# Performance work log

Hardware: AMD Instinct MI355X
Metric: run time of the kernel (lower is better)

The kernel has to match this reference:

```python
import jax, jax.numpy as jnp
import numpy as np

EPS_POS = 0.65
EPS_NEG = 0.4
TAU = 0.03
TEMPERATURE = 0.07


def setup_inputs() -> dict:
    key = jax.random.key(0)
    k1, k2 = jax.random.split(key)
    N, H, W, C = 256, 14, 14, 512  # ResNet18 layer4 features (448x448 frame), pooled audio
    frame = jax.random.normal(k1, (N, H, W, C), dtype=jnp.float32)
    audio = jax.random.normal(k2, (N, C), dtype=jnp.float32)
    return {"frame": frame, "audio": audio}


def reference(frame, audio):
    # frame: [N, H, W, C] vision backbone features; audio: [N, C] pooled audio embedding
    N = frame.shape[0]
    f = frame * jax.lax.rsqrt(jnp.sum(frame * frame, axis=3, keepdims=True))  # l2_normalize axis=3
    a = audio * jax.lax.rsqrt(jnp.sum(audio * audio, axis=1, keepdims=True))  # l2_normalize axis=1

    # S_ii: per-sample spatial similarity map [N, 1, H, W]
    S_ii = jnp.einsum('nhwc,nc->nhw', f, a)[:, None, :, :]
    # S_ij: cross-batch similarity [N, K, H, W] (K == N)
    S_ij = jnp.einsum('nhwc,kc->nkhw', f, a)

    m_ip = jax.nn.sigmoid((S_ii - EPS_POS) / TAU)   # positive soft-mask
    neg = 1.0 - jax.nn.sigmoid((S_ii - EPS_NEG) / TAU)  # hard-negative soft-mask

    # Pi: masked mean of positive similarities -> [N, 1]
    Pi = jnp.sum(m_ip * S_ii, axis=(2, 3)) / jnp.sum(m_ip, axis=(2, 3))

    n_all = jax.nn.sigmoid((S_ij - EPS_POS) / TAU)
    mask = 1.0 - 100.0 * jnp.eye(N, dtype=frame.dtype)  # kill diagonal (self) pairs
    Ni_easy = (jnp.sum(n_all * S_ij, axis=(2, 3)) / jnp.sum(n_all, axis=(2, 3))) * mask  # [N, N]
    Ni_hard = jnp.sum(neg * S_ii, axis=(2, 3)) / jnp.sum(neg, axis=(2, 3))  # [N, 1]

    data = jnp.concatenate([Pi, Ni_hard, Ni_easy], axis=1) * TEMPERATURE  # [N, N+2]

    # __calc_loss (faithful to TF broadcasting: Pi_d is [N,1], Ni_d is [N] -> [N,N] broadcast)
    Pi_d = data[:, 0:1]
    Ni_d = jnp.sum(data[:, 1:], axis=1)
    Pi_e = jnp.exp(Pi_d)
    Ni_e = jnp.exp(Ni_d)
    loss = (-1.0 / N) * jnp.sum(jnp.log(Pi_e / (Pi_e + Ni_e)))
    return loss
```

## Files before the change

### kernel.cpp

```cpp
#include <hip/hip_runtime.h>
#include <stdint.h>

#define N_IMG 256
#define HW 196
#define CDIM 512

#define F_EPS_POS 0.65f
#define F_EPS_NEG 0.40f
#define F_INV_TAU (1.0f/0.03f)
#define F_TEMP 0.07f

typedef __attribute__((ext_vector_type(8))) short bf16x8;
typedef __attribute__((ext_vector_type(4))) unsigned short u16x4;
typedef __attribute__((ext_vector_type(4))) float f32x4;

__device__ __forceinline__ unsigned short f2bf(float x){
    unsigned int u = __float_as_uint(x);
    u = (u + 0x7FFFu + ((u >> 16) & 1u)) >> 16;
    return (unsigned short)u;
}
__device__ __forceinline__ float sigm(float x){ return 1.0f/(1.0f + __expf(-x)); }

__global__ void audio_norm_k(const float* __restrict__ audio,
                             unsigned short* __restrict__ abf){
    int k = blockIdx.x, t = threadIdx.x;
    __shared__ float red[256];
    float v0 = audio[k*CDIM + t];
    float v1 = audio[k*CDIM + t + 256];
    red[t] = v0*v0 + v1*v1;
    __syncthreads();
    for (int s = 128; s > 0; s >>= 1){
        if (t < s) red[t] += red[t+s];
        __syncthreads();
    }
    float rrt = 1.0f / sqrtf(red[0]);
    abf[k*CDIM + t]       = f2bf(v0*rrt);
    abf[k*CDIM + t + 256] = f2bf(v1*rrt);
}

__global__ __launch_bounds__(512, 2)
void main_k(const float* __restrict__ frame,
            const unsigned short* __restrict__ abf,
            float* __restrict__ num, float* __restrict__ den,
            float* __restrict__ hnum, float* __restrict__ hden){
    __shared__ unsigned short fT[2][16*520];
    __shared__ float rnormS[2][16];

    const int t    = threadIdx.x;
    const int n    = blockIdx.x;
    const int lane = t & 63, wid = t >> 6;
    const int col  = lane & 15, quad = lane >> 4;
    const int kg0  = wid*32 + col;
    const int kg1  = kg0 + 16;

    bf16x8 B0[16], B1[16];
    {
        const unsigned short* b0p = abf + (size_t)kg0*CDIM + quad*8;
        const unsigned short* b1p = abf + (size_t)kg1*CDIM + quad*8;
        #pragma unroll
        for (int j = 0; j < 16; ++j){
            B0[j] = *(const bf16x8*)(b0p + j*32);
            B1[j] = *(const bf16x8*)(b1p + j*32);
        }
    }

    const int r0 = 2*wid, r1 = r0 + 1;

    float en0=0.f, en1=0.f, ed0=0.f, ed1=0.f;
    float hn0=0.f, hn1=0.f, hd0=0.f, hd1=0.f;

    auto loadT = [&](int pt, float4* v){
        int p0 = pt*16 + r0; if (p0 > HW-1) p0 = HW-1;
        int p1 = pt*16 + r1; if (p1 > HW-1) p1 = HW-1;
        const float4* s0 = (const float4*)(frame + ((size_t)n*HW + p0)*CDIM);
        const float4* s1 = (const float4*)(frame + ((size_t)n*HW + p1)*CDIM);
        v[0] = s0[lane]; v[1] = s0[lane + 64];
        v[2] = s1[lane]; v[3] = s1[lane + 64];
    };
    auto storeT = [&](const float4* v, int buf){
        float ss0 = v[0].x*v[0].x + v[0].y*v[0].y + v[0].z*v[0].z + v[0].w*v[0].w
                  + v[1].x*v[1].x + v[1].y*v[1].y + v[1].z*v[1].z + v[1].w*v[1].w;
        float ss1 = v[2].x*v[2].x + v[2].y*v[2].y + v[2].z*v[2].z + v[2].w*v[2].w
                  + v[3].x*v[3].x + v[3].y*v[3].y + v[3].z*v[3].z + v[3].w*v[3].w;
        unsigned short* d0 = fT[buf] + r0*520;
        unsigned short* d1 = fT[buf] + r1*520;
        u16x4 u0 = { f2bf(v[0].x), f2bf(v[0].y), f2bf(v[0].z), f2bf(v[0].w) };
        u16x4 u1 = { f2bf(v[1].x), f2bf(v[1].y), f2bf(v[1].z), f2bf(v[1].w) };
        u16x4 u2 = { f2bf(v[2].x), f2bf(v[2].y), f2bf(v[2].z), f2bf(v[2].w) };
        u16x4 u3 = { f2bf(v[3].x), f2bf(v[3].y), f2bf(v[3].z), f2bf(v[3].w) };
        *(u16x4*)(d0 + lane*4)       = u0;
        *(u16x4*)(d0 + 256 + lane*4) = u1;
        *(u16x4*)(d1 + lane*4)       = u2;
        *(u16x4*)(d1 + 256 + lane*4) = u3;
        #pragma unroll
        for (int d = 1; d < 64; d <<= 1){
            ss0 += __shfl_xor(ss0, d, 64);
            ss1 += __shfl_xor(ss1, d, 64);
        }
        if (lane == 0){
            rnormS[buf][r0] = (ss0 > 0.f) ? (1.0f/sqrtf(ss0)) : 0.f;
            rnormS[buf][r1] = (ss1 > 0.f) ? (1.0f/sqrtf(ss1)) : 0.f;
        }
    };

    {
        float4 v[4];
        loadT(0, v);
        storeT(v, 0);
    }
    __syncthreads();

    for (int pt = 0; pt < 13; ++pt){
        const int cur = pt & 1, nxt = cur ^ 1;
        const bool hasNext = (pt < 12);

        float4 v[4];
        if (hasNext) loadT(pt + 1, v);

        const unsigned short* fbase = fT[cur] + col*520 + quad*8;
        f32x4 acc0 = {0.f,0.f,0.f,0.f};
        f32x4 acc1 = {0.f,0.f,0.f,0.f};
        #pragma unroll
        for (int j = 0; j < 16; ++j){
            bf16x8 a = *(const bf16x8*)(fbase + j*32);
            acc0 = __builtin_amdgcn_mfma_f32_16x16x32_bf16(a, B0[j], acc0, 0, 0, 0);
            acc1 = __builtin_amdgcn_mfma_f32_16x16x32_bf16(a, B1[j], acc1, 0, 0, 0);
        }
        f32x4 rn4 = *(const f32x4*)(&rnormS[cur][quad*4]);
        #pragma unroll
        for (int rr = 0; rr < 4; ++rr){
            int prow = pt*16 + quad*4 + rr;
            if (prow < HW){
                float s0 = acc0[rr] * rn4[rr];
                float s1 = acc1[rr] * rn4[rr];
                float w0 = sigm((s0 - F_EPS_POS) * F_INV_TAU);
                float w1 = sigm((s1 - F_EPS_POS) * F_INV_TAU);
                en0 += w0*s0; ed0 += w0;
                en1 += w1*s1; ed1 += w1;
                if (kg0 == n){ float wn = 1.f - sigm((s0 - F_EPS_NEG) * F_INV_TAU); hn0 += wn*s0; hd0 += wn; }
                if (kg1 == n){ float wn = 1.f - sigm((s1 - F_EPS_NEG) * F_INV_TAU); hn1 += wn*s1; hd1 += wn; }
            }
        }

        if (hasNext) storeT(v, nxt);
        __syncthreads();
    }

    en0 += __shfl_xor(en0, 16, 64); en0 += __shfl_xor(en0, 32, 64);
    ed0 += __shfl_xor(ed0, 16, 64); ed0 += __shfl_xor(ed0, 32, 64);
    en1 += __shfl_xor(en1, 16, 64); en1 += __shfl_xor(en1, 32, 64);
    ed1 += __shfl_xor(ed1, 16, 64); ed1 += __shfl_xor(ed1, 32, 64);
    hn0 += __shfl_xor(hn0, 16, 64); hn0 += __shfl_xor(hn0, 32, 64);
    hd0 += __shfl_xor(hd0, 16, 64); hd0 += __shfl_xor(hd0, 32, 64);
    hn1 += __shfl_xor(hn1, 16, 64); hn1 += __shfl_xor(hn1, 32, 64);
    hd1 += __shfl_xor(hd1, 16, 64); hd1 += __shfl_xor(hd1, 32, 64);

    if (quad == 0){
        num[n*N_IMG + kg0] = en0;  den[n*N_IMG + kg0] = ed0;
        num[n*N_IMG + kg1] = en1;  den[n*N_IMG + kg1] = ed1;
        if (kg0 == n){ hnum[n] = hn0; hden[n] = hd0; }
        if (kg1 == n){ hnum[n] = hn1; hden[n] = hd1; }
    }
}

__global__ void pd_k(const float* __restrict__ num, const float* __restrict__ den,
                     const float* __restrict__ hnum, const float* __restrict__ hden,
                     float* __restrict__ Pi_d, float* __restrict__ Ni_d){
    int nn = blockIdx.x, t = threadIdx.x;
    __shared__ float red[256];
    __shared__ float diagv;
    float ratio = num[nn*N_IMG + t] / den[nn*N_IMG + t];
    if (t == nn) diagv = ratio;
    red[t] = ratio * (t == nn ? -99.f : 1.f);
    __syncthreads();
    for (int s = 128; s > 0; s >>= 1){
        if (t < s) red[t] += red[t+s];
        __syncthreads();
    }
    if (t == 0){
        Pi_d[nn] = F_TEMP * diagv;
        Ni_d[nn] = F_TEMP * (hnum[nn]/hden[nn] + red[0]);
    }
}

__global__ void loss_k(const float* __restrict__ Pi_d, const float* __restrict__ Ni_d,
                       float* __restrict__ out){
    int i = blockIdx.x, j = threadIdx.x;
    __shared__ float red[256];
    float x = Ni_d[j] - Pi_d[i];
    red[j] = (x > 20.f) ? x : log1pf(__expf(x));
    __syncthreads();
    for (int s = 128; s > 0; s >>= 1){
        if (j < s) red[j] += red[j+s];
        __syncthreads();
    }
    if (j == 0) atomicAdd(out, red[0] * (1.0f/(float)N_IMG));
}

extern "C" void kernel_launch(void* const* d_in, const int* in_sizes, int n_in,
                              void* d_out, int out_size, void* d_ws, size_t ws_size,
                              hipStream_t stream) {
    const float* frame = (const float*)d_in[0];
    const float* audio = (const float*)d_in[1];
    float* out = (float*)d_out;
    char* ws = (char*)d_ws;

    unsigned short* abf = (unsigned short*)(ws);
    float* num  = (float*)(ws + 262144);
    float* den  = (float*)(ws + 524288);
    float* hnum = (float*)(ws + 786432);
    float* hden = (float*)(ws + 787456);
    float* Pi_d = (float*)(ws + 788480);
    float* Ni_d = (float*)(ws + 789504);

    hipMemsetAsync(out, 0, sizeof(float), stream);

    audio_norm_k<<<N_IMG, 256, 0, stream>>>(audio, abf);
    main_k<<<N_IMG, 512, 0, stream>>>(frame, abf, num, den, hnum, hden);
    pd_k<<<N_IMG, 256, 0, stream>>>(num, den, hnum, hden, Pi_d, Ni_d);
    loss_k<<<N_IMG, 256, 0, stream>>>(Pi_d, Ni_d, out);
}
```

Baseline: 175.9 us.

## Deepen global prefetch to two tiles and replace syncthreads with LDS-only barrier

The frame tile loop is fully unrolled and uses two register buffers, so global loads for tile pt+2 are issued while tile pt is computed and tile pt+1 is stored to LDS. __syncthreads is replaced by a barrier that waits only on LDS counters, so outstanding global loads do not stall at each barrier. This is meant to hide HBM latency in the memory-bound main kernel. In exchange it raises register pressure under a launch bound of 2 blocks per CU, which could cause spills.

```diff
diff --git a/kernel.cpp b/kernel.cpp
--- a/kernel.cpp
+++ b/kernel.cpp
@@ -69,11 +69,13 @@
     float en0=0.f, en1=0.f, ed0=0.f, ed1=0.f;
     float hn0=0.f, hn1=0.f, hd0=0.f, hd1=0.f;
 
+    const float4* fbase_g = (const float4*)(frame + (size_t)n*HW*CDIM);
+
     auto loadT = [&](int pt, float4* v){
         int p0 = pt*16 + r0; if (p0 > HW-1) p0 = HW-1;
         int p1 = pt*16 + r1; if (p1 > HW-1) p1 = HW-1;
-        const float4* s0 = (const float4*)(frame + ((size_t)n*HW + p0)*CDIM);
-        const float4* s1 = (const float4*)(frame + ((size_t)n*HW + p1)*CDIM);
+        const float4* s0 = fbase_g + (size_t)p0*(CDIM/4);
+        const float4* s1 = fbase_g + (size_t)p1*(CDIM/4);
         v[0] = s0[lane]; v[1] = s0[lane + 64];
         v[2] = s1[lane]; v[3] = s1[lane + 64];
     };
@@ -93,9 +95,9 @@
         *(u16x4*)(d1 + lane*4)       = u2;
         *(u16x4*)(d1 + 256 + lane*4) = u3;
         #pragma unroll
-        for (int d = 1; d < 64; d <<= 1){
-            ss0 += __shfl_xor(ss0, d, 64);
-            ss1 += __shfl_xor(ss1, d, 64);
+        for (int dd = 1; dd < 64; dd <<= 1){
+            ss0 += __shfl_xor(ss0, dd, 64);
+            ss1 += __shfl_xor(ss1, dd, 64);
         }
         if (lane == 0){
             rnormS[buf][r0] = (ss0 > 0.f) ? (1.0f/sqrtf(ss0)) : 0.f;
@@ -103,48 +105,65 @@
         }
     };
 
-    {
-        float4 v[4];
-        loadT(0, v);
-        storeT(v, 0);
-    }
-    __syncthreads();
-
-    for (int pt = 0; pt < 13; ++pt){
-        const int cur = pt & 1, nxt = cur ^ 1;
-        const bool hasNext = (pt < 12);
-
-        float4 v[4];
-        if (hasNext) loadT(pt + 1, v);
-
-        const unsigned short* fbase = fT[cur] + col*520 + quad*8;
-        f32x4 acc0 = {0.f,0.f,0.f,0.f};
-        f32x4 acc1 = {0.f,0.f,0.f,0.f};
-        #pragma unroll
-        for (int j = 0; j < 16; ++j){
-            bf16x8 a = *(const bf16x8*)(fbase + j*32);
-            acc0 = __builtin_amdgcn_mfma_f32_16x16x32_bf16(a, B0[j], acc0, 0, 0, 0);
-            acc1 = __builtin_amdgcn_mfma_f32_16x16x32_bf16(a, B1[j], acc1, 0, 0, 0);
-        }
-        f32x4 rn4 = *(const f32x4*)(&rnormS[cur][quad*4]);
-        #pragma unroll
-        for (int rr = 0; rr < 4; ++rr){
-            int prow = pt*16 + quad*4 + rr;
-            if (prow < HW){
-                float s0 = acc0[rr] * rn4[rr];
-                float s1 = acc1[rr] * rn4[rr];
-                float w0 = sigm((s0 - F_EPS_POS) * F_INV_TAU);
-                float w1 = sigm((s1 - F_EPS_POS) * F_INV_TAU);
-                en0 += w0*s0; ed0 += w0;
-                en1 += w1*s1; ed1 += w1;
-                if (kg0 == n){ float wn = 1.f - sigm((s0 - F_EPS_NEG) * F_INV_TAU); hn0 += wn*s0; hd0 += wn; }
-                if (kg1 == n){ float wn = 1.f - sigm((s1 - F_EPS_NEG) * F_INV_TAU); hn1 += wn*s1; hd1 += wn; }
-            }
-        }
-
-        if (hasNext) storeT(v, nxt);
-        __syncthreads();
-    }
+    auto soft_barrier = [&](){
+        asm volatile("s_waitcnt lgkmcnt(0)" ::: "memory");
+        __builtin_amdgcn_s_barrier();
+    };
+
+    float4 vA[4], vB[4];
+
+    loadT(0, vA);
+    storeT(vA, 0);
+    loadT(1, vA);
+    soft_barrier();
+
+#define BODY(PT, P, Q) do{                                                     \
+    if ((PT)+2 < 13) loadT((PT)+2, Q);                                         \
+    __builtin_amdgcn_sched_barrier(0);     \
+    {                                                                          \
+        const unsigned short* fb = fT[(PT)&1] + col*520 + quad*8;              \
+        f32x4 acc0 = {0.f,0.f,0.f,0.f};                                        \
+        f32x4 acc1 = {0.f,0.f,0.f,0.f};                                        \
+        _Pragma("unroll")                                                      \
+        for (int j = 0; j < 16; ++j){                                          \
+            bf16x8 a = *(const bf16x8*)(fb + j*32);                            \
+            acc0 = __builtin_amdgcn_mfma_f32_16x16x32_bf16(a, B0[j], acc0, 0,0,0);\
+            acc1 = __builtin_amdgcn_mfma_f32_16x16x32_bf16(a, B1[j], acc1, 0,0,0);\
+        }                                                                      \
+        f32x4 rn4 = *(const f32x4*)(&rnormS[(PT)&1][quad*4]);                  \
+        _Pragma("unroll")                                                      \
+        for (int rr = 0; rr < 4; ++rr){                                        \
+            int prow = (PT)*16 + quad*4 + rr;                                  \
+            if (prow < HW){                                                    \
+                float s0 = acc0[rr] * rn4[rr];                                 \
+                float s1 = acc1[rr] * rn4[rr];                                 \
+                float w0 = sigm((s0 - F_EPS_POS) * F_INV_TAU);                 \
+                float w1 = sigm((s1 - F_EPS_POS) * F_INV_TAU);                 \
+                en0 += w0*s0; ed0 += w0;                                       \
+                en1 += w1*s1; ed1 += w1;                                       \
+                if (kg0 == n){ float wn = 1.f - sigm((s0 - F_EPS_NEG) * F_INV_TAU); hn0 += wn*s0; hd0 += wn; } \
+                if (kg1 == n){ float wn = 1.f - sigm((s1 - F_EPS_NEG) * F_INV_TAU); hn1 += wn*s1; hd1 += wn; } \
+            }                                                                  \
+        }                                                                      \
+    }                                                                          \
+    if ((PT)+1 < 13) storeT(P, ((PT)+1)&1);       \
+    soft_barrier();                                                            \
+}while(0)
+
+    BODY(0,  vA, vB);
+    BODY(1,  vB, vA);
+    BODY(2,  vA, vB);
+    BODY(3,  vB, vA);
+    BODY(4,  vA, vB);
+    BODY(5,  vB, vA);
+    BODY(6,  vA, vB);
+    BODY(7,  vB, vA);
+    BODY(8,  vA, vB);
+    BODY(9,  vB, vA);
+    BODY(10, vA, vB);
+    BODY(11, vB, vA);
+    BODY(12, vA, vB);
+#undef BODY
 
     en0 += __shfl_xor(en0, 16, 64); en0 += __shfl_xor(en0, 32, 64);
     ed0 += __shfl_xor(ed0, 16, 64); ed0 += __shfl_xor(ed0, 32, 64);
```

Result: slower. 181.9 us (+3.4%).

## Pre-normalize frame to bf16 in separate kernel and stream tiles via direct-to-LDS loads

Applied to the files above, without the earlier changes.

Adds a highly parallel fnorm kernel that converts the frame to bf16 in workspace, using an XOR-swizzled row layout, and stores per-pixel reciprocal norms. The main kernel then stages 16-row tiles with global_load_lds straight into shared memory instead of loading fp32 into registers, converting and storing. This takes conversion work and register round-trips out of the latency-bound per-image loop and halves the bytes the main kernel reads. In exchange it adds an extra 51 MB bf16 write and read through HBM, plus one more kernel launch.

```diff
diff --git a/kernel.cpp b/kernel.cpp
--- a/kernel.cpp
+++ b/kernel.cpp
@@ -4,6 +4,7 @@
 #define N_IMG 256
 #define HW 196
 #define CDIM 512
+#define RSTRIDE 208
 
 #define F_EPS_POS 0.65f
 #define F_EPS_NEG 0.40f
@@ -38,13 +39,37 @@
     abf[k*CDIM + t + 256] = f2bf(v1*rrt);
 }
 
+__global__ __launch_bounds__(512)
+void fnorm_k(const float* __restrict__ frame,
+             unsigned short* __restrict__ fbf,
+             float* __restrict__ rnorm){
+    const int lane = threadIdx.x & 63, wid = threadIdx.x >> 6;
+    const int p = blockIdx.x * 8 + wid;
+    const int n = blockIdx.y;
+    if (p >= HW) return;
+    const float4* src = (const float4*)(frame + ((size_t)n*HW + p)*CDIM);
+    float4 a = src[lane], b = src[lane + 64];
+    float ss = a.x*a.x + a.y*a.y + a.z*a.z + a.w*a.w
+             + b.x*b.x + b.y*b.y + b.z*b.z + b.w*b.w;
+    #pragma unroll
+    for (int d = 1; d < 64; d <<= 1) ss += __shfl_xor(ss, d, 64);
+    char* dst = (char*)(fbf + ((size_t)n*HW + p)*CDIM);
+    u16x4 u0 = { f2bf(a.x), f2bf(a.y), f2bf(a.z), f2bf(a.w) };
+    u16x4 u1 = { f2bf(b.x), f2bf(b.y), f2bf(b.z), f2bf(b.w) };
+    const int sw = (p & 3) << 4;
+    *(u16x4*)(dst + (((lane*8) ^ sw)))         = u0;
+    *(u16x4*)(dst + (512 + ((lane*8) ^ sw)))   = u1;
+    if (lane == 0)
+        rnorm[(size_t)n*RSTRIDE + p] = (ss > 0.f) ? (1.0f/sqrtf(ss)) : 0.f;
+}
+
 __global__ __launch_bounds__(512, 2)
-void main_k(const float* __restrict__ frame,
+void main_k(const unsigned short* __restrict__ fbf,
+            const float* __restrict__ rnorm,
             const unsigned short* __restrict__ abf,
             float* __restrict__ num, float* __restrict__ den,
             float* __restrict__ hnum, float* __restrict__ hden){
-    __shared__ unsigned short fT[2][16*520];
-    __shared__ float rnormS[2][16];
+    __shared__ unsigned short fT[2][16*CDIM];
 
     const int t    = threadIdx.x;
     const int n    = blockIdx.x;
@@ -65,68 +90,45 @@
     }
 
     const int r0 = 2*wid, r1 = r0 + 1;
+    const char* gbase = (const char*)(fbf + (size_t)n*HW*CDIM);
 
     float en0=0.f, en1=0.f, ed0=0.f, ed1=0.f;
     float hn0=0.f, hn1=0.f, hd0=0.f, hd1=0.f;
 
-    auto loadT = [&](int pt, float4* v){
+    auto stage = [&](int pt, int buf){
         int p0 = pt*16 + r0; if (p0 > HW-1) p0 = HW-1;
         int p1 = pt*16 + r1; if (p1 > HW-1) p1 = HW-1;
-        const float4* s0 = (const float4*)(frame + ((size_t)n*HW + p0)*CDIM);
-        const float4* s1 = (const float4*)(frame + ((size_t)n*HW + p1)*CDIM);
-        v[0] = s0[lane]; v[1] = s0[lane + 64];
-        v[2] = s1[lane]; v[3] = s1[lane + 64];
+        const char* s0 = gbase + (size_t)p0*(CDIM*2) + lane*16;
+        const char* s1 = gbase + (size_t)p1*(CDIM*2) + lane*16;
+        __builtin_amdgcn_global_load_lds(
+            (const __attribute__((address_space(1))) void*)s0,
+            (__attribute__((address_space(3))) void*)&fT[buf][r0*CDIM], 16, 0, 0);
+        __builtin_amdgcn_global_load_lds(
+            (const __attribute__((address_space(1))) void*)s1,
+            (__attribute__((address_space(3))) void*)&fT[buf][r1*CDIM], 16, 0, 0);
     };
-    auto storeT = [&](const float4* v, int buf){
-        float ss0 = v[0].x*v[0].x + v[0].y*v[0].y + v[0].z*v[0].z + v[0].w*v[0].w
-                  + v[1].x*v[1].x + v[1].y*v[1].y + v[1].z*v[1].z + v[1].w*v[1].w;
-        float ss1 = v[2].x*v[2].x + v[2].y*v[2].y + v[2].z*v[2].z + v[2].w*v[2].w
-                  + v[3].x*v[3].x + v[3].y*v[3].y + v[3].z*v[3].z + v[3].w*v[3].w;
-        unsigned short* d0 = fT[buf] + r0*520;
-        unsigned short* d1 = fT[buf] + r1*520;
-        u16x4 u0 = { f2bf(v[0].x), f2bf(v[0].y), f2bf(v[0].z), f2bf(v[0].w) };
-        u16x4 u1 = { f2bf(v[1].x), f2bf(v[1].y), f2bf(v[1].z), f2bf(v[1].w) };
-        u16x4 u2 = { f2bf(v[2].x), f2bf(v[2].y), f2bf(v[2].z), f2bf(v[2].w) };
-        u16x4 u3 = { f2bf(v[3].x), f2bf(v[3].y), f2bf(v[3].z), f2bf(v[3].w) };
-        *(u16x4*)(d0 + lane*4)       = u0;
-        *(u16x4*)(d0 + 256 + lane*4) = u1;
-        *(u16x4*)(d1 + lane*4)       = u2;
-        *(u16x4*)(d1 + 256 + lane*4) = u3;
-        #pragma unroll
-        for (int d = 1; d < 64; d <<= 1){
-            ss0 += __shfl_xor(ss0, d, 64);
-            ss1 += __shfl_xor(ss1, d, 64);
-        }
-        if (lane == 0){
-            rnormS[buf][r0] = (ss0 > 0.f) ? (1.0f/sqrtf(ss0)) : 0.f;
-            rnormS[buf][r1] = (ss1 > 0.f) ? (1.0f/sqrtf(ss1)) : 0.f;
-        }
-    };
-
-    {
-        float4 v[4];
-        loadT(0, v);
-        storeT(v, 0);
-    }
-    __syncthreads();
+
+    stage(0, 0);
+    __syncthreads();
+
+    const unsigned short* fb0 = (const unsigned short*)
+        ((const char*)fT[0] + col*1024 + ((quad ^ (col & 3)) << 4));
+    const unsigned short* fb1 = (const unsigned short*)
+        ((const char*)fT[1] + col*1024 + ((quad ^ (col & 3)) << 4));
 
     for (int pt = 0; pt < 13; ++pt){
-        const int cur = pt & 1, nxt = cur ^ 1;
-        const bool hasNext = (pt < 12);
-
-        float4 v[4];
-        if (hasNext) loadT(pt + 1, v);
-
-        const unsigned short* fbase = fT[cur] + col*520 + quad*8;
+        if (pt < 12) stage(pt + 1, (pt + 1) & 1);
+
+        const unsigned short* fb = (pt & 1) ? fb1 : fb0;
         f32x4 acc0 = {0.f,0.f,0.f,0.f};
         f32x4 acc1 = {0.f,0.f,0.f,0.f};
         #pragma unroll
         for (int j = 0; j < 16; ++j){
-            bf16x8 a = *(const bf16x8*)(fbase + j*32);
+            bf16x8 a = *(const bf16x8*)(fb + j*32);
             acc0 = __builtin_amdgcn_mfma_f32_16x16x32_bf16(a, B0[j], acc0, 0, 0, 0);
             acc1 = __builtin_amdgcn_mfma_f32_16x16x32_bf16(a, B1[j], acc1, 0, 0, 0);
         }
-        f32x4 rn4 = *(const f32x4*)(&rnormS[cur][quad*4]);
+        f32x4 rn4 = *(const f32x4*)(rnorm + (size_t)n*RSTRIDE + pt*16 + quad*4);
         #pragma unroll
         for (int rr = 0; rr < 4; ++rr){
             int prow = pt*16 + quad*4 + rr;
@@ -141,8 +143,6 @@
                 if (kg1 == n){ float wn = 1.f - sigm((s1 - F_EPS_NEG) * F_INV_TAU); hn1 += wn*s1; hd1 += wn; }
             }
         }
-
-        if (hasNext) storeT(v, nxt);
         __syncthreads();
     }
 
@@ -205,18 +205,21 @@
     float* out = (float*)d_out;
     char* ws = (char*)d_ws;
 
-    unsigned short* abf = (unsigned short*)(ws);
-    float* num  = (float*)(ws + 262144);
-    float* den  = (float*)(ws + 524288);
-    float* hnum = (float*)(ws + 786432);
-    float* hden = (float*)(ws + 787456);
-    float* Pi_d = (float*)(ws + 788480);
-    float* Ni_d = (float*)(ws + 789504);
+    unsigned short* abf   = (unsigned short*)(ws);
+    unsigned short* fbf   = (unsigned short*)(ws + 262144);
+    float*          rnorm = (float*)(ws + 51642368);
+    float*          num   = (float*)(ws + 51855360);
+    float*          den   = (float*)(ws + 52117504);
+    float*          hnum  = (float*)(ws + 52379648);
+    float*          hden  = (float*)(ws + 52380672);
+    float*          Pi_d  = (float*)(ws + 52381696);
+    float*          Ni_d  = (float*)(ws + 52382720);
 
     hipMemsetAsync(out, 0, sizeof(float), stream);
 
     audio_norm_k<<<N_IMG, 256, 0, stream>>>(audio, abf);
-    main_k<<<N_IMG, 512, 0, stream>>>(frame, abf, num, den, hnum, hden);
+    fnorm_k<<<dim3(25, N_IMG), 512, 0, stream>>>(frame, fbf, rnorm);
+    main_k<<<N_IMG, 512, 0, stream>>>(fbf, rnorm, abf, num, den, hnum, hden);
     pd_k<<<N_IMG, 256, 0, stream>>>(num, den, hnum, hden, Pi_d, Ni_d);
     loss_k<<<N_IMG, 256, 0, stream>>>(Pi_d, Ni_d, out);
 }
```

New measurement: 201.3 us. 14.4% more time.

## Split audio columns across two blocks per image to double grid size

Applied to the files above, without the earlier changes.

Each frame image is now processed by two blocks, and each block handles half of the 256 audio columns. Each wave keeps one B fragment set and one accumulator instead of two, so register use drops and launch bounds allow 4 blocks per CU. This raises occupancy and parallelism on a 256-CU device, where 256 blocks left little latency hiding. The cost is that every frame tile is read from global memory and converted to bf16 twice, doubling frame traffic and the normalization work.

```diff
diff --git a/kernel.cpp b/kernel.cpp
--- a/kernel.cpp
+++ b/kernel.cpp
@@ -38,7 +38,7 @@
     abf[k*CDIM + t + 256] = f2bf(v1*rrt);
 }
 
-__global__ __launch_bounds__(512, 2)
+__global__ __launch_bounds__(512, 4)
 void main_k(const float* __restrict__ frame,
             const unsigned short* __restrict__ abf,
             float* __restrict__ num, float* __restrict__ den,
@@ -47,33 +47,30 @@
     __shared__ float rnormS[2][16];
 
     const int t    = threadIdx.x;
-    const int n    = blockIdx.x;
+    const int n    = blockIdx.x & 255;
+    const int kh   = blockIdx.x >> 8;
     const int lane = t & 63, wid = t >> 6;
     const int col  = lane & 15, quad = lane >> 4;
-    const int kg0  = wid*32 + col;
-    const int kg1  = kg0 + 16;
-
-    bf16x8 B0[16], B1[16];
+    const int kg   = kh*128 + wid*16 + col;
+
+    bf16x8 B[16];
     {
-        const unsigned short* b0p = abf + (size_t)kg0*CDIM + quad*8;
-        const unsigned short* b1p = abf + (size_t)kg1*CDIM + quad*8;
-        #pragma unroll
-        for (int j = 0; j < 16; ++j){
-            B0[j] = *(const bf16x8*)(b0p + j*32);
-            B1[j] = *(const bf16x8*)(b1p + j*32);
-        }
+        const unsigned short* bp = abf + (size_t)kg*CDIM + quad*8;
+        #pragma unroll
+        for (int j = 0; j < 16; ++j) B[j] = *(const bf16x8*)(bp + j*32);
     }
 
     const int r0 = 2*wid, r1 = r0 + 1;
 
-    float en0=0.f, en1=0.f, ed0=0.f, ed1=0.f;
-    float hn0=0.f, hn1=0.f, hd0=0.f, hd1=0.f;
+    float en = 0.f, ed = 0.f, hn = 0.f, hd = 0.f;
+
+    const float4* fbase_g = (const float4*)(frame + (size_t)n*HW*CDIM);
 
     auto loadT = [&](int pt, float4* v){
         int p0 = pt*16 + r0; if (p0 > HW-1) p0 = HW-1;
         int p1 = pt*16 + r1; if (p1 > HW-1) p1 = HW-1;
-        const float4* s0 = (const float4*)(frame + ((size_t)n*HW + p0)*CDIM);
-        const float4* s1 = (const float4*)(frame + ((size_t)n*HW + p1)*CDIM);
+        const float4* s0 = fbase_g + (size_t)p0*(CDIM/4);
+        const float4* s1 = fbase_g + (size_t)p1*(CDIM/4);
         v[0] = s0[lane]; v[1] = s0[lane + 64];
         v[2] = s1[lane]; v[3] = s1[lane + 64];
     };
@@ -93,9 +90,9 @@
         *(u16x4*)(d1 + lane*4)       = u2;
         *(u16x4*)(d1 + 256 + lane*4) = u3;
         #pragma unroll
-        for (int d = 1; d < 64; d <<= 1){
-            ss0 += __shfl_xor(ss0, d, 64);
-            ss1 += __shfl_xor(ss1, d, 64);
+        for (int dd = 1; dd < 64; dd <<= 1){
+            ss0 += __shfl_xor(ss0, dd, 64);
+            ss1 += __shfl_xor(ss1, dd, 64);
         }
         if (lane == 0){
             rnormS[buf][r0] = (ss0 > 0.f) ? (1.0f/sqrtf(ss0)) : 0.f;
@@ -118,27 +115,21 @@
         if (hasNext) loadT(pt + 1, v);
 
         const unsigned short* fbase = fT[cur] + col*520 + quad*8;
-        f32x4 acc0 = {0.f,0.f,0.f,0.f};
-        f32x4 acc1 = {0.f,0.f,0.f,0.f};
+        f32x4 acc = {0.f,0.f,0.f,0.f};
         #pragma unroll
         for (int j = 0; j < 16; ++j){
             bf16x8 a = *(const bf16x8*)(fbase + j*32);
-            acc0 = __builtin_amdgcn_mfma_f32_16x16x32_bf16(a, B0[j], acc0, 0, 0, 0);
-            acc1 = __builtin_amdgcn_mfma_f32_16x16x32_bf16(a, B1[j], acc1, 0, 0, 0);
+            acc = __builtin_amdgcn_mfma_f32_16x16x32_bf16(a, B[j], acc, 0, 0, 0);
         }
         f32x4 rn4 = *(const f32x4*)(&rnormS[cur][quad*4]);
         #pragma unroll
         for (int rr = 0; rr < 4; ++rr){
             int prow = pt*16 + quad*4 + rr;
             if (prow < HW){
-                float s0 = acc0[rr] * rn4[rr];
-                float s1 = acc1[rr] * rn4[rr];
-                float w0 = sigm((s0 - F_EPS_POS) * F_INV_TAU);
-                float w1 = sigm((s1 - F_EPS_POS) * F_INV_TAU);
-                en0 += w0*s0; ed0 += w0;
-                en1 += w1*s1; ed1 += w1;
-                if (kg0 == n){ float wn = 1.f - sigm((s0 - F_EPS_NEG) * F_INV_TAU); hn0 += wn*s0; hd0 += wn; }
-                if (kg1 == n){ float wn = 1.f - sigm((s1 - F_EPS_NEG) * F_INV_TAU); hn1 += wn*s1; hd1 += wn; }
+                float s  = acc[rr] * rn4[rr];
+                float wp = sigm((s - F_EPS_POS) * F_INV_TAU);
+                en += wp*s; ed += wp;
+                if (kg == n){ float wn = 1.f - sigm((s - F_EPS_NEG) * F_INV_TAU); hn += wn*s; hd += wn; }
             }
         }
 
@@ -146,20 +137,14 @@
         __syncthreads();
     }
 
-    en0 += __shfl_xor(en0, 16, 64); en0 += __shfl_xor(en0, 32, 64);
-    ed0 += __shfl_xor(ed0, 16, 64); ed0 += __shfl_xor(ed0, 32, 64);
-    en1 += __shfl_xor(en1, 16, 64); en1 += __shfl_xor(en1, 32, 64);
-    ed1 += __shfl_xor(ed1, 16, 64); ed1 += __shfl_xor(ed1, 32, 64);
-    hn0 += __shfl_xor(hn0, 16, 64); hn0 += __shfl_xor(hn0, 32, 64);
-    hd0 += __shfl_xor(hd0, 16, 64); hd0 += __shfl_xor(hd0, 32, 64);
-    hn1 += __shfl_xor(hn1, 16, 64); hn1 += __shfl_xor(hn1, 32, 64);
-    hd1 += __shfl_xor(hd1, 16, 64); hd1 += __shfl_xor(hd1, 32, 64);
+    en += __shfl_xor(en, 16, 64); en += __shfl_xor(en, 32, 64);
+    ed += __shfl_xor(ed, 16, 64); ed += __shfl_xor(ed, 32, 64);
+    hn += __shfl_xor(hn, 16, 64); hn += __shfl_xor(hn, 32, 64);
+    hd += __shfl_xor(hd, 16, 64); hd += __shfl_xor(hd, 32, 64);
 
     if (quad == 0){
-        num[n*N_IMG + kg0] = en0;  den[n*N_IMG + kg0] = ed0;
-        num[n*N_IMG + kg1] = en1;  den[n*N_IMG + kg1] = ed1;
-        if (kg0 == n){ hnum[n] = hn0; hden[n] = hd0; }
-        if (kg1 == n){ hnum[n] = hn1; hden[n] = hd1; }
+        num[n*N_IMG + kg] = en;  den[n*N_IMG + kg] = ed;
+        if (kg == n){ hnum[n] = hn; hden[n] = hd; }
     }
 }
 
@@ -216,7 +201,7 @@
     hipMemsetAsync(out, 0, sizeof(float), stream);
 
     audio_norm_k<<<N_IMG, 256, 0, stream>>>(audio, abf);
-    main_k<<<N_IMG, 512, 0, stream>>>(frame, abf, num, den, hnum, hden);
+    main_k<<<N_IMG*2, 512, 0, stream>>>(frame, abf, num, den, hnum, hden);
     pd_k<<<N_IMG, 256, 0, stream>>>(num, den, hnum, hden, Pi_d, Ni_d);
     loss_k<<<N_IMG, 256, 0, stream>>>(Pi_d, Ni_d, out);
 }
```

After: 175.6 us. Within noise of the previous version (-0.2%).
